# Kernel optimization log

Hardware: AMD Instinct MI355X
Metric: run time of the kernel (lower is better)

The kernel has to match this reference:

```python
import jax, jax.numpy as jnp
import numpy as np


def setup_inputs() -> dict:
    key = jax.random.key(0)
    k = jax.random.split(key, 5)
    B, S, D, H = 4, 2048, 2048, 8192
    scale1 = 1.0 / np.sqrt(D)
    scale2 = 1.0 / np.sqrt(H)
    return {
        "x": jax.random.normal(k[0], (B, S, D), dtype=jnp.float32),
        "w1": jax.random.normal(k[1], (H, D), dtype=jnp.float32) * scale1,
        "b1": jax.random.normal(k[2], (H,), dtype=jnp.float32) * scale1,
        "w2": jax.random.normal(k[3], (D, H), dtype=jnp.float32) * scale2,
        "b2": jax.random.normal(k[4], (D,), dtype=jnp.float32) * scale2,
    }


def reference(x, w1, b1, w2, b2):
    # fc1: [B,S,D] @ [D,H] -> [B,S,H]
    h = jnp.einsum("bsd,hd->bsh", x, w1) + b1
    # squared ReLU activation
    a = jnp.square(jax.nn.relu(h))
    # fc2: [B,S,H] @ [H,D] -> [B,S,D]
    return jnp.einsum("bsh,dh->bsd", a, w2) + b2
```

## Files before the change

### kernel.cpp

```cpp
#include <hip/hip_runtime.h>
#include <hip/hip_bf16.h>
#include <stdint.h>

typedef __bf16 bf16x8 __attribute__((ext_vector_type(8)));
typedef float f32x4 __attribute__((ext_vector_type(4)));


__device__ inline void gload_lds16(const void* g, void* lds) {
  __builtin_amdgcn_global_load_lds(
      (const __attribute__((address_space(1))) uint32_t*)(uintptr_t)g,
      (__attribute__((address_space(3))) uint32_t*)(uintptr_t)lds,
      16, 0, 0);
}

#define DSR(dst, base, OFF)                                         \
  asm volatile("ds_read_b128 %0, %1 offset:" #OFF                   \
               : "=v"(dst) : "v"(base))

#define LGKM(N) do {                                             \
    asm volatile("s_waitcnt lgkmcnt(" #N ")" ::: "memory");      \
    __builtin_amdgcn_sched_barrier(0);                           \
  } while (0)
#define VM(N) do {                                               \
    asm volatile("s_waitcnt vmcnt(" #N ")" ::: "memory");        \
    __builtin_amdgcn_sched_barrier(0);                           \
  } while (0)

__device__ inline short f2bf(float f) {
  union { float f; uint32_t u; } x; x.f = f;
  uint32_t u = x.u;
  u += 0x7fffu + ((u >> 16) & 1u);
  return (short)(u >> 16);
}

#define BAR() do { asm volatile("" ::: "memory"); \
                   __builtin_amdgcn_s_barrier();  \
                   asm volatile("" ::: "memory"); } while (0)


__global__ __launch_bounds__(256) void cvt_f32_bf16(
    const float* __restrict__ in, short* __restrict__ out, int n4) {
  int i = blockIdx.x * 256 + threadIdx.x;
  if (i < n4) {
    float4 v = reinterpret_cast<const float4*>(in)[i];
    short4 o;
    o.x = f2bf(v.x); o.y = f2bf(v.y); o.z = f2bf(v.z); o.w = f2bf(v.w);
    reinterpret_cast<short4*>(out)[i] = o;
  }
}


template <int EPI>
__global__ __launch_bounds__(512, 2) void gemm_bt(
    const short* __restrict__ A, const short* __restrict__ B,
    const float* __restrict__ bias, void* __restrict__ Cout,
    int M, int N, int K) {
  __shared__ __align__(16) short lds[2][4][128 * 64];

  const int tid  = threadIdx.x;
  const int wave = tid >> 6;
  const int lane = tid & 63;
  const int wr = wave >> 2;
  const int wc = wave & 3;
  const int fr = lane & 15, kq = lane >> 4;

  const int nwg = gridDim.x;
  const int w = (blockIdx.x & 7) * (nwg >> 3) + (blockIdx.x >> 3);
  const int gy = M >> 8;
  const int brow = w % gy;
  const int bcol = w / gy;

  f32x4 acc[8][4];
#pragma unroll
  for (int m = 0; m < 8; ++m)
#pragma unroll
    for (int n = 0; n < 4; ++n)
      acc[m][n] = (f32x4){0.f, 0.f, 0.f, 0.f};

  const int nk = K >> 6;

  const uint32_t LB = (uint32_t)(uintptr_t)&lds[0][0][0];
  uint32_t bA[2], bB[2];
  {
    const uint32_t x0 = (uint32_t)(((kq)     ^ (fr & 7)) * 16);
    const uint32_t x1 = (uint32_t)(((4 + kq) ^ (fr & 7)) * 16);
    const uint32_t ra = (uint32_t)((wr * 64 + fr) * 128);
    const uint32_t rb = (uint32_t)((wc * 32 + fr) * 128);
    bA[0] = LB + ra + x0;            bA[1] = LB + ra + x1;
    bB[0] = LB + 32768u + rb + x0;   bB[1] = LB + 32768u + rb + x1;
  }

  const int i0 = tid;
  const int gl0 = i0 ^ ((i0 >> 3) & 7);
  const int r0 = gl0 >> 3, c0 = gl0 & 7;
  const size_t rstep = (size_t)128 * K;

  const short* pA[2];
  const short* pB[2];
  {
    const int rb0 = (r0 >> 5) * 64 + (r0 & 31);
#pragma unroll
    for (int h = 0; h < 2; ++h) {
      pA[h] = A + (size_t)(brow * 256 + h * 64 + r0) * K + c0 * 8;
      pB[h] = B + (size_t)(bcol * 256 + rb0 + h * 32) * K + c0 * 8;
    }
  }

  const int dst0 = wave * 512, dst1 = 4096 + wave * 512;

#define STAGE(p, buf, slot)                              \
  do {                                                   \
    short* base_ = &lds[buf][slot][0];                   \
    gload_lds16((p), base_ + dst0);                      \
    gload_lds16((p) + rstep, base_ + dst1);              \
    (p) += 64;                                           \
  } while (0)

  bf16x8 a0q[4][2], a1q[4][2], bq0[2][2], bq1[2][2];
  auto Q1 = [&]() {
#pragma unroll
    for (int m = 0; m < 4; ++m)
#pragma unroll
      for (int n = 0; n < 2; ++n)
#pragma unroll
        for (int kk = 0; kk < 2; ++kk)
          acc[m][n] = __builtin_amdgcn_mfma_f32_16x16x32_bf16(
              bq0[n][kk], a0q[m][kk], acc[m][n], 0, 0, 0);
  };
  auto Q2 = [&]() {
#pragma unroll
    for (int m = 0; m < 4; ++m)
#pragma unroll
      for (int n = 0; n < 2; ++n)
#pragma unroll
        for (int kk = 0; kk < 2; ++kk)
          acc[m][n + 2] = __builtin_amdgcn_mfma_f32_16x16x32_bf16(
              bq1[n][kk], a0q[m][kk], acc[m][n + 2], 0, 0, 0);
  };
  auto Q3 = [&]() {
#pragma unroll
    for (int m = 0; m < 4; ++m)
#pragma unroll
      for (int n = 0; n < 2; ++n)
#pragma unroll
        for (int kk = 0; kk < 2; ++kk)
          acc[m + 4][n + 2] = __builtin_amdgcn_mfma_f32_16x16x32_bf16(
              bq1[n][kk], a1q[m][kk], acc[m + 4][n + 2], 0, 0, 0);
  };
  auto Q4 = [&]() {
#pragma unroll
    for (int m = 0; m < 4; ++m)
#pragma unroll
      for (int n = 0; n < 2; ++n)
#pragma unroll
        for (int kk = 0; kk < 2; ++kk)
          acc[m + 4][n] = __builtin_amdgcn_mfma_f32_16x16x32_bf16(
              bq0[n][kk], a1q[m][kk], acc[m + 4][n], 0, 0, 0);
  };

#define PRIO_ON  __builtin_amdgcn_s_setprio(1)
#define PRIO_OFF __builtin_amdgcn_s_setprio(0)

  STAGE(pA[0], 0, 0);
  STAGE(pB[0], 0, 2);
  STAGE(pB[1], 0, 3);
  STAGE(pA[1], 0, 1);
  STAGE(pA[0], 1, 0);
  STAGE(pB[0], 1, 2);
  STAGE(pB[1], 1, 3);
  VM(6);
  BAR();

  for (int t = 0; t < nk; ++t) {
    const int cur = t & 1, nxt = cur ^ 1;
    const bool s1 = (t + 1) < nk, g2 = (t + 2) < nk;
    if (t) {
      const int32_t d = cur ? 65536 : -65536;
      bA[0] += d; bA[1] += d; bB[0] += d; bB[1] += d;
    }

    DSR(a0q[0][0], bA[0], 0);     DSR(a0q[0][1], bA[1], 0);
    DSR(a0q[1][0], bA[0], 2048);  DSR(a0q[1][1], bA[1], 2048);
    DSR(a0q[2][0], bA[0], 4096);  DSR(a0q[2][1], bA[1], 4096);
    DSR(a0q[3][0], bA[0], 6144);  DSR(a0q[3][1], bA[1], 6144);
    DSR(bq0[0][0], bB[0], 0);     DSR(bq0[0][1], bB[1], 0);
    DSR(bq0[1][0], bB[0], 2048);  DSR(bq0[1][1], bB[1], 2048);
    if (s1) STAGE(pA[1], nxt, 1);
    LGKM(8);
    BAR();
    LGKM(0);
    PRIO_ON; Q1(); PRIO_OFF;
    BAR();

    DSR(bq1[0][0], bB[0], 16384); DSR(bq1[0][1], bB[1], 16384);
    DSR(bq1[1][0], bB[0], 18432); DSR(bq1[1][1], bB[1], 18432);
    if (g2) STAGE(pA[0], cur, 0);
    BAR();
    LGKM(0);
    PRIO_ON; Q2(); PRIO_OFF;
    BAR();

    DSR(a1q[0][0], bA[0], 16384); DSR(a1q[0][1], bA[1], 16384);
    DSR(a1q[1][0], bA[0], 18432); DSR(a1q[1][1], bA[1], 18432);
    DSR(a1q[2][0], bA[0], 20480); DSR(a1q[2][1], bA[1], 20480);
    DSR(a1q[3][0], bA[0], 22528); DSR(a1q[3][1], bA[1], 22528);
    if (g2) STAGE(pB[0], cur, 2);
    BAR();
    LGKM(0);
    PRIO_ON; Q3(); PRIO_OFF;
    BAR();

    if (g2) STAGE(pB[1], cur, 3);
    BAR();
    PRIO_ON; Q4(); PRIO_OFF;
    if (g2)      { VM(6); }
    else if (s1) { VM(0); }
    if (s1) BAR();
  }

  const int q = lane >> 4;
  if (EPI == 0) {
    short* C = (short*)Cout;
#pragma unroll
    for (int m = 0; m < 8; ++m) {
      const int row = brow * 256 + wr * 128 + m * 16 + fr;
#pragma unroll
      for (int n = 0; n < 4; ++n) {
        const int col = bcol * 256 + wc * 64 + n * 16 + q * 4;
        const float4 bv = *(const float4*)&bias[col];
        short4 o;
        float v0 = acc[m][n][0] + bv.x; v0 = v0 > 0.f ? v0 * v0 : 0.f;
        float v1 = acc[m][n][1] + bv.y; v1 = v1 > 0.f ? v1 * v1 : 0.f;
        float v2 = acc[m][n][2] + bv.z; v2 = v2 > 0.f ? v2 * v2 : 0.f;
        float v3 = acc[m][n][3] + bv.w; v3 = v3 > 0.f ? v3 * v3 : 0.f;
        o.x = f2bf(v0); o.y = f2bf(v1); o.z = f2bf(v2); o.w = f2bf(v3);
        *(short4*)&C[(size_t)row * N + col] = o;
      }
    }
  } else {
    float* C = (float*)Cout;
#pragma unroll
    for (int m = 0; m < 8; ++m) {
      const int row = brow * 256 + wr * 128 + m * 16 + fr;
#pragma unroll
      for (int n = 0; n < 4; ++n) {
        const int col = bcol * 256 + wc * 64 + n * 16 + q * 4;
        const float4 bv = *(const float4*)&bias[col];
        float4 o;
        o.x = acc[m][n][0] + bv.x;
        o.y = acc[m][n][1] + bv.y;
        o.z = acc[m][n][2] + bv.z;
        o.w = acc[m][n][3] + bv.w;
        *(float4*)&C[(size_t)row * N + col] = o;
      }
    }
  }
#undef STAGE
}


extern "C" void kernel_launch(void* const* d_in, const int* in_sizes, int n_in,
                              void* d_out, int out_size, void* d_ws,
                              size_t ws_size, hipStream_t stream) {
  const float* x  = (const float*)d_in[0];
  const float* w1 = (const float*)d_in[1];
  const float* b1 = (const float*)d_in[2];
  const float* w2 = (const float*)d_in[3];
  const float* b2 = (const float*)d_in[4];
  float* out = (float*)d_out;

  const int H = in_sizes[2];
  const int D = in_sizes[4];
  const int M = in_sizes[0] / D;

  short* xb  = (short*)d_ws;
  short* w1b = xb  + (size_t)M * D;
  short* w2b = w1b + (size_t)H * D;
  short* act = w2b + (size_t)D * H;

  {
    int n4 = (M * D) / 4;
    cvt_f32_bf16<<<(n4 + 255) / 256, 256, 0, stream>>>(x, xb, n4);
    n4 = (H * D) / 4;
    cvt_f32_bf16<<<(n4 + 255) / 256, 256, 0, stream>>>(w1, w1b, n4);
    n4 = (D * H) / 4;
    cvt_f32_bf16<<<(n4 + 255) / 256, 256, 0, stream>>>(w2, w2b, n4);
  }

  gemm_bt<0><<<(M / 256) * (H / 256), 512, 0, stream>>>(
      xb, w1b, b1, (void*)act, M, H, D);
  gemm_bt<1><<<(M / 256) * (D / 256), 512, 0, stream>>>(
      act, w2b, b2, (void*)out, M, D, H);
}
```

Before: 547.9 us.

## Unroll GEMM main loop by two with cross-iteration LDS fragment prefetch

Restructures the double-buffered bf16 MFMA main loop into a two-way unrolled loop with ping-pong register sets, so the first A/B fragments of the next K-tile are read from LDS during the last quadrant of the current tile. It uses fixed per-buffer LDS base addresses instead of runtime toggling, and moves global-to-LDS staging and vmcnt waits into a uniform schedule with a peeled tail. The aim is to hide LDS read latency behind MFMA work and cut per-iteration branch and address arithmetic. The cost is more VGPRs for the extra fragment set, which may lower occupancy. The loop also assumes an even number of K-tiles.

```diff
diff --git a/kernel.cpp b/kernel.cpp
--- a/kernel.cpp
+++ b/kernel.cpp
@@ -80,14 +80,16 @@
   const int nk = K >> 6;
 
   const uint32_t LB = (uint32_t)(uintptr_t)&lds[0][0][0];
-  uint32_t bA[2], bB[2];
+  uint32_t bA0[2], bB0[2], bA1[2], bB1[2];
   {
     const uint32_t x0 = (uint32_t)(((kq)     ^ (fr & 7)) * 16);
     const uint32_t x1 = (uint32_t)(((4 + kq) ^ (fr & 7)) * 16);
     const uint32_t ra = (uint32_t)((wr * 64 + fr) * 128);
     const uint32_t rb = (uint32_t)((wc * 32 + fr) * 128);
-    bA[0] = LB + ra + x0;            bA[1] = LB + ra + x1;
-    bB[0] = LB + 32768u + rb + x0;   bB[1] = LB + 32768u + rb + x1;
+    bA0[0] = LB + ra + x0;            bA0[1] = LB + ra + x1;
+    bB0[0] = LB + 32768u + rb + x0;   bB0[1] = LB + 32768u + rb + x1;
+    bA1[0] = bA0[0] + 65536u;         bA1[1] = bA0[1] + 65536u;
+    bB1[0] = bB0[0] + 65536u;         bB1[1] = bB0[1] + 65536u;
   }
 
   const int i0 = tid;
@@ -116,8 +118,30 @@
     (p) += 64;                                           \
   } while (0)
 
-  bf16x8 a0q[4][2], a1q[4][2], bq0[2][2], bq1[2][2];
-  auto Q1 = [&]() {
+  bf16x8 a0X[4][2], b0X[2][2], a0Y[4][2], b0Y[2][2];
+  bf16x8 a1q[4][2], b1q[2][2];
+
+  auto PRE = [&](bf16x8 (&aS)[4][2], bf16x8 (&bS)[2][2],
+                 const uint32_t* bA_, const uint32_t* bB_) {
+    DSR(aS[0][0], bA_[0], 0);     DSR(aS[0][1], bA_[1], 0);
+    DSR(aS[1][0], bA_[0], 2048);  DSR(aS[1][1], bA_[1], 2048);
+    DSR(aS[2][0], bA_[0], 4096);  DSR(aS[2][1], bA_[1], 4096);
+    DSR(aS[3][0], bA_[0], 6144);  DSR(aS[3][1], bA_[1], 6144);
+    DSR(bS[0][0], bB_[0], 0);     DSR(bS[0][1], bB_[1], 0);
+    DSR(bS[1][0], bB_[0], 2048);  DSR(bS[1][1], bB_[1], 2048);
+  };
+  auto RDB1 = [&](const uint32_t* bB_) {
+    DSR(b1q[0][0], bB_[0], 16384); DSR(b1q[0][1], bB_[1], 16384);
+    DSR(b1q[1][0], bB_[0], 18432); DSR(b1q[1][1], bB_[1], 18432);
+  };
+  auto RDA1 = [&](const uint32_t* bA_) {
+    DSR(a1q[0][0], bA_[0], 16384); DSR(a1q[0][1], bA_[1], 16384);
+    DSR(a1q[1][0], bA_[0], 18432); DSR(a1q[1][1], bA_[1], 18432);
+    DSR(a1q[2][0], bA_[0], 20480); DSR(a1q[2][1], bA_[1], 20480);
+    DSR(a1q[3][0], bA_[0], 22528); DSR(a1q[3][1], bA_[1], 22528);
+  };
+
+  auto Q1 = [&](bf16x8 (&aS)[4][2], bf16x8 (&bS)[2][2]) {
 #pragma unroll
     for (int m = 0; m < 4; ++m)
 #pragma unroll
@@ -125,9 +149,9 @@
 #pragma unroll
         for (int kk = 0; kk < 2; ++kk)
           acc[m][n] = __builtin_amdgcn_mfma_f32_16x16x32_bf16(
-              bq0[n][kk], a0q[m][kk], acc[m][n], 0, 0, 0);
-  };
-  auto Q2 = [&]() {
+              bS[n][kk], aS[m][kk], acc[m][n], 0, 0, 0);
+  };
+  auto Q2 = [&](bf16x8 (&aS)[4][2]) {
 #pragma unroll
     for (int m = 0; m < 4; ++m)
 #pragma unroll
@@ -135,7 +159,7 @@
 #pragma unroll
         for (int kk = 0; kk < 2; ++kk)
           acc[m][n + 2] = __builtin_amdgcn_mfma_f32_16x16x32_bf16(
-              bq1[n][kk], a0q[m][kk], acc[m][n + 2], 0, 0, 0);
+              b1q[n][kk], aS[m][kk], acc[m][n + 2], 0, 0, 0);
   };
   auto Q3 = [&]() {
 #pragma unroll
@@ -145,9 +169,9 @@
 #pragma unroll
         for (int kk = 0; kk < 2; ++kk)
           acc[m + 4][n + 2] = __builtin_amdgcn_mfma_f32_16x16x32_bf16(
-              bq1[n][kk], a1q[m][kk], acc[m + 4][n + 2], 0, 0, 0);
-  };
-  auto Q4 = [&]() {
+              b1q[n][kk], a1q[m][kk], acc[m + 4][n + 2], 0, 0, 0);
+  };
+  auto Q4 = [&](bf16x8 (&bS)[2][2]) {
 #pragma unroll
     for (int m = 0; m < 4; ++m)
 #pragma unroll
@@ -155,7 +179,7 @@
 #pragma unroll
         for (int kk = 0; kk < 2; ++kk)
           acc[m + 4][n] = __builtin_amdgcn_mfma_f32_16x16x32_bf16(
-              bq0[n][kk], a1q[m][kk], acc[m + 4][n], 0, 0, 0);
+              bS[n][kk], a1q[m][kk], acc[m + 4][n], 0, 0, 0);
   };
 
 #define PRIO_ON  __builtin_amdgcn_s_setprio(1)
@@ -170,53 +194,75 @@
   STAGE(pB[1], 1, 3);
   VM(6);
   BAR();
-
-  for (int t = 0; t < nk; ++t) {
-    const int cur = t & 1, nxt = cur ^ 1;
-    const bool s1 = (t + 1) < nk, g2 = (t + 2) < nk;
-    if (t) {
-      const int32_t d = cur ? 65536 : -65536;
-      bA[0] += d; bA[1] += d; bB[0] += d; bB[1] += d;
-    }
-
-    DSR(a0q[0][0], bA[0], 0);     DSR(a0q[0][1], bA[1], 0);
-    DSR(a0q[1][0], bA[0], 2048);  DSR(a0q[1][1], bA[1], 2048);
-    DSR(a0q[2][0], bA[0], 4096);  DSR(a0q[2][1], bA[1], 4096);
-    DSR(a0q[3][0], bA[0], 6144);  DSR(a0q[3][1], bA[1], 6144);
-    DSR(bq0[0][0], bB[0], 0);     DSR(bq0[0][1], bB[1], 0);
-    DSR(bq0[1][0], bB[0], 2048);  DSR(bq0[1][1], bB[1], 2048);
-    if (s1) STAGE(pA[1], nxt, 1);
+  PRE(a0X, b0X, bA0, bB0);
+
+  const int niter = nk >> 1;
+  for (int i = 0; i < niter - 1; ++i) {
+    RDB1(bB0);  STAGE(pA[1], 1, 1);
+    BAR(); LGKM(4);
+    PRIO_ON; Q1(a0X, b0X); PRIO_OFF;
+    VM(8); BAR();
+    RDA1(bA0);  STAGE(pA[0], 0, 0);
+    BAR(); LGKM(8);
+    PRIO_ON; Q2(a0X); PRIO_OFF;
+    VM(8); BAR();
+    STAGE(pB[0], 0, 2);
+    BAR(); LGKM(0);
+    PRIO_ON; Q3(); PRIO_OFF;
+    VM(8); BAR();
+    PRE(a0Y, b0Y, bA1, bB1);  STAGE(pB[1], 0, 3);
     LGKM(8);
-    BAR();
-    LGKM(0);
-    PRIO_ON; Q1(); PRIO_OFF;
-    BAR();
-
-    DSR(bq1[0][0], bB[0], 16384); DSR(bq1[0][1], bB[1], 16384);
-    DSR(bq1[1][0], bB[0], 18432); DSR(bq1[1][1], bB[1], 18432);
-    if (g2) STAGE(pA[0], cur, 0);
-    BAR();
-    LGKM(0);
-    PRIO_ON; Q2(); PRIO_OFF;
-    BAR();
-
-    DSR(a1q[0][0], bA[0], 16384); DSR(a1q[0][1], bA[1], 16384);
-    DSR(a1q[1][0], bA[0], 18432); DSR(a1q[1][1], bA[1], 18432);
-    DSR(a1q[2][0], bA[0], 20480); DSR(a1q[2][1], bA[1], 20480);
-    DSR(a1q[3][0], bA[0], 22528); DSR(a1q[3][1], bA[1], 22528);
-    if (g2) STAGE(pB[0], cur, 2);
-    BAR();
-    LGKM(0);
+    BAR(); __builtin_amdgcn_sched_barrier(0);
+    PRIO_ON; Q4(b0X); PRIO_OFF;
+    VM(8); BAR();
+
+    RDB1(bB1);  STAGE(pA[1], 0, 1);
+    BAR(); LGKM(4);
+    PRIO_ON; Q1(a0Y, b0Y); PRIO_OFF;
+    VM(8); BAR();
+    RDA1(bA1);  STAGE(pA[0], 1, 0);
+    BAR(); LGKM(8);
+    PRIO_ON; Q2(a0Y); PRIO_OFF;
+    VM(8); BAR();
+    STAGE(pB[0], 1, 2);
+    BAR(); LGKM(0);
     PRIO_ON; Q3(); PRIO_OFF;
-    BAR();
-
-    if (g2) STAGE(pB[1], cur, 3);
-    BAR();
-    PRIO_ON; Q4(); PRIO_OFF;
-    if (g2)      { VM(6); }
-    else if (s1) { VM(0); }
-    if (s1) BAR();
-  }
+    VM(8); BAR();
+    PRE(a0X, b0X, bA0, bB0);  STAGE(pB[1], 1, 3);
+    LGKM(8);
+    BAR(); __builtin_amdgcn_sched_barrier(0);
+    PRIO_ON; Q4(b0Y); PRIO_OFF;
+    VM(8); BAR();
+  }
+
+  RDB1(bB0);  STAGE(pA[1], 1, 1);
+  BAR(); LGKM(4);
+  PRIO_ON; Q1(a0X, b0X); PRIO_OFF;
+  VM(0); BAR();
+  RDA1(bA0);
+  BAR(); LGKM(8);
+  PRIO_ON; Q2(a0X); PRIO_OFF;
+  BAR();
+  BAR(); LGKM(0);
+  PRIO_ON; Q3(); PRIO_OFF;
+  BAR();
+  PRE(a0Y, b0Y, bA1, bB1);
+  LGKM(8);
+  BAR(); __builtin_amdgcn_sched_barrier(0);
+  PRIO_ON; Q4(b0X); PRIO_OFF;
+  BAR();
+  RDB1(bB1);
+  BAR(); LGKM(4);
+  PRIO_ON; Q1(a0Y, b0Y); PRIO_OFF;
+  BAR();
+  RDA1(bA1);
+  BAR(); LGKM(8);
+  PRIO_ON; Q2(a0Y); PRIO_OFF;
+  BAR();
+  BAR(); LGKM(0);
+  PRIO_ON; Q3(); PRIO_OFF;
+  BAR();
+  PRIO_ON; Q4(b0Y); PRIO_OFF;
 
   const int q = lane >> 4;
   if (EPI == 0) {
```

After: 2.183 ms. 3.98x slower.

## Use 4-wave 256-thread GEMM blocks with 128x128 per-wave tiles and unrolled double-buffer loop

Applied to the files above, without the earlier changes.

Cuts the GEMM workgroup from 8 waves to 4. Each wave now computes a 128x128 output tile (8x8 accumulators) instead of 128x64, which raises register reuse of LDS fragments per MFMA. The main loop is unrolled by two over the double buffer so buffer indices and LDS addresses are constants, and a peeled epilogue drains the pipeline with explicit vmcnt waits. Each wave now issues four global-to-LDS loads per stage, and the doubled accumulator set with occupancy bound 1 risks register spills and less latency hiding.

```diff
diff --git a/kernel.cpp b/kernel.cpp
--- a/kernel.cpp
+++ b/kernel.cpp
@@ -51,7 +51,7 @@
 
 
 template <int EPI>
-__global__ __launch_bounds__(512, 2) void gemm_bt(
+__global__ __launch_bounds__(256, 1) void gemm_bt(
     const short* __restrict__ A, const short* __restrict__ B,
     const float* __restrict__ bias, void* __restrict__ Cout,
     int M, int N, int K) {
@@ -60,8 +60,8 @@
   const int tid  = threadIdx.x;
   const int wave = tid >> 6;
   const int lane = tid & 63;
-  const int wr = wave >> 2;
-  const int wc = wave & 3;
+  const int wr = wave >> 1;
+  const int wc = wave & 1;
   const int fr = lane & 15, kq = lane >> 4;
 
   const int nwg = gridDim.x;
@@ -70,58 +70,58 @@
   const int brow = w % gy;
   const int bcol = w / gy;
 
-  f32x4 acc[8][4];
+  f32x4 acc[8][8];
 #pragma unroll
   for (int m = 0; m < 8; ++m)
 #pragma unroll
-    for (int n = 0; n < 4; ++n)
+    for (int n = 0; n < 8; ++n)
       acc[m][n] = (f32x4){0.f, 0.f, 0.f, 0.f};
 
   const int nk = K >> 6;
 
   const uint32_t LB = (uint32_t)(uintptr_t)&lds[0][0][0];
-  uint32_t bA[2], bB[2];
+  uint32_t bA0[2], bB0[2], bA1b[2], bB1b[2];
   {
     const uint32_t x0 = (uint32_t)(((kq)     ^ (fr & 7)) * 16);
     const uint32_t x1 = (uint32_t)(((4 + kq) ^ (fr & 7)) * 16);
     const uint32_t ra = (uint32_t)((wr * 64 + fr) * 128);
-    const uint32_t rb = (uint32_t)((wc * 32 + fr) * 128);
-    bA[0] = LB + ra + x0;            bA[1] = LB + ra + x1;
-    bB[0] = LB + 32768u + rb + x0;   bB[1] = LB + 32768u + rb + x1;
-  }
-
-  const int i0 = tid;
-  const int gl0 = i0 ^ ((i0 >> 3) & 7);
+    const uint32_t rb = (uint32_t)((wc * 64 + fr) * 128);
+    bA0[0] = LB + ra + x0;            bA0[1] = LB + ra + x1;
+    bB0[0] = LB + 32768u + rb + x0;   bB0[1] = LB + 32768u + rb + x1;
+    bA1b[0] = bA0[0] + 65536u;        bA1b[1] = bA0[1] + 65536u;
+    bB1b[0] = bB0[0] + 65536u;        bB1b[1] = bB0[1] + 65536u;
+  }
+
+  const int gl0 = (tid ^ ((tid >> 3) & 7)) & 255;
   const int r0 = gl0 >> 3, c0 = gl0 & 7;
-  const size_t rstep = (size_t)128 * K;
 
   const short* pA[2];
   const short* pB[2];
-  {
-    const int rb0 = (r0 >> 5) * 64 + (r0 & 31);
-#pragma unroll
-    for (int h = 0; h < 2; ++h) {
-      pA[h] = A + (size_t)(brow * 256 + h * 64 + r0) * K + c0 * 8;
-      pB[h] = B + (size_t)(bcol * 256 + rb0 + h * 32) * K + c0 * 8;
-    }
-  }
-
-  const int dst0 = wave * 512, dst1 = 4096 + wave * 512;
-
-#define STAGE(p, buf, slot)                              \
-  do {                                                   \
-    short* base_ = &lds[buf][slot][0];                   \
-    gload_lds16((p), base_ + dst0);                      \
-    gload_lds16((p) + rstep, base_ + dst1);              \
-    (p) += 64;                                           \
+#pragma unroll
+  for (int s = 0; s < 2; ++s) {
+    pA[s] = A + (size_t)(brow * 256 + s * 64 + r0) * K + c0 * 8;
+    pB[s] = B + (size_t)(bcol * 256 + s * 64 + r0) * K + c0 * 8;
+  }
+  const size_t rk32 = (size_t)32 * K, rk128 = (size_t)128 * K;
+  const size_t rk160 = (size_t)160 * K;
+  const int dstw = wave * 512;
+
+#define STAGE(p, buf, slot)                                       \
+  do {                                                            \
+    short* base_ = &lds[buf][slot][0];                            \
+    gload_lds16((p),          base_ + dstw);                      \
+    gload_lds16((p) + rk32,   base_ + 2048 + dstw);               \
+    gload_lds16((p) + rk128,  base_ + 4096 + dstw);               \
+    gload_lds16((p) + rk160,  base_ + 6144 + dstw);               \
+    (p) += 64;                                                    \
   } while (0)
 
-  bf16x8 a0q[4][2], a1q[4][2], bq0[2][2], bq1[2][2];
+  bf16x8 a0q[4][2], a1q[4][2], bq0[4][2], bq1[4][2];
   auto Q1 = [&]() {
 #pragma unroll
     for (int m = 0; m < 4; ++m)
 #pragma unroll
-      for (int n = 0; n < 2; ++n)
+      for (int n = 0; n < 4; ++n)
 #pragma unroll
         for (int kk = 0; kk < 2; ++kk)
           acc[m][n] = __builtin_amdgcn_mfma_f32_16x16x32_bf16(
@@ -131,31 +131,55 @@
 #pragma unroll
     for (int m = 0; m < 4; ++m)
 #pragma unroll
-      for (int n = 0; n < 2; ++n)
+      for (int n = 0; n < 4; ++n)
 #pragma unroll
         for (int kk = 0; kk < 2; ++kk)
-          acc[m][n + 2] = __builtin_amdgcn_mfma_f32_16x16x32_bf16(
-              bq1[n][kk], a0q[m][kk], acc[m][n + 2], 0, 0, 0);
+          acc[m][n + 4] = __builtin_amdgcn_mfma_f32_16x16x32_bf16(
+              bq1[n][kk], a0q[m][kk], acc[m][n + 4], 0, 0, 0);
   };
   auto Q3 = [&]() {
 #pragma unroll
     for (int m = 0; m < 4; ++m)
 #pragma unroll
-      for (int n = 0; n < 2; ++n)
+      for (int n = 0; n < 4; ++n)
 #pragma unroll
         for (int kk = 0; kk < 2; ++kk)
-          acc[m + 4][n + 2] = __builtin_amdgcn_mfma_f32_16x16x32_bf16(
-              bq1[n][kk], a1q[m][kk], acc[m + 4][n + 2], 0, 0, 0);
+          acc[m + 4][n + 4] = __builtin_amdgcn_mfma_f32_16x16x32_bf16(
+              bq1[n][kk], a1q[m][kk], acc[m + 4][n + 4], 0, 0, 0);
   };
   auto Q4 = [&]() {
 #pragma unroll
     for (int m = 0; m < 4; ++m)
 #pragma unroll
-      for (int n = 0; n < 2; ++n)
+      for (int n = 0; n < 4; ++n)
 #pragma unroll
         for (int kk = 0; kk < 2; ++kk)
           acc[m + 4][n] = __builtin_amdgcn_mfma_f32_16x16x32_bf16(
               bq0[n][kk], a1q[m][kk], acc[m + 4][n], 0, 0, 0);
+  };
+  auto RD_A0 = [&](const uint32_t* bA_) {
+    DSR(a0q[0][0], bA_[0], 0);     DSR(a0q[0][1], bA_[1], 0);
+    DSR(a0q[1][0], bA_[0], 2048);  DSR(a0q[1][1], bA_[1], 2048);
+    DSR(a0q[2][0], bA_[0], 4096);  DSR(a0q[2][1], bA_[1], 4096);
+    DSR(a0q[3][0], bA_[0], 6144);  DSR(a0q[3][1], bA_[1], 6144);
+  };
+  auto RD_B0 = [&](const uint32_t* bB_) {
+    DSR(bq0[0][0], bB_[0], 0);     DSR(bq0[0][1], bB_[1], 0);
+    DSR(bq0[1][0], bB_[0], 2048);  DSR(bq0[1][1], bB_[1], 2048);
+    DSR(bq0[2][0], bB_[0], 4096);  DSR(bq0[2][1], bB_[1], 4096);
+    DSR(bq0[3][0], bB_[0], 6144);  DSR(bq0[3][1], bB_[1], 6144);
+  };
+  auto RD_B1 = [&](const uint32_t* bB_) {
+    DSR(bq1[0][0], bB_[0], 16384); DSR(bq1[0][1], bB_[1], 16384);
+    DSR(bq1[1][0], bB_[0], 18432); DSR(bq1[1][1], bB_[1], 18432);
+    DSR(bq1[2][0], bB_[0], 20480); DSR(bq1[2][1], bB_[1], 20480);
+    DSR(bq1[3][0], bB_[0], 22528); DSR(bq1[3][1], bB_[1], 22528);
+  };
+  auto RD_A1 = [&](const uint32_t* bA_) {
+    DSR(a1q[0][0], bA_[0], 16384); DSR(a1q[0][1], bA_[1], 16384);
+    DSR(a1q[1][0], bA_[0], 18432); DSR(a1q[1][1], bA_[1], 18432);
+    DSR(a1q[2][0], bA_[0], 20480); DSR(a1q[2][1], bA_[1], 20480);
+    DSR(a1q[3][0], bA_[0], 22528); DSR(a1q[3][1], bA_[1], 22528);
   };
 
 #define PRIO_ON  __builtin_amdgcn_s_setprio(1)
@@ -168,55 +192,78 @@
   STAGE(pA[0], 1, 0);
   STAGE(pB[0], 1, 2);
   STAGE(pB[1], 1, 3);
-  VM(6);
+  VM(12);
   BAR();
 
-  for (int t = 0; t < nk; ++t) {
-    const int cur = t & 1, nxt = cur ^ 1;
-    const bool s1 = (t + 1) < nk, g2 = (t + 2) < nk;
-    if (t) {
-      const int32_t d = cur ? 65536 : -65536;
-      bA[0] += d; bA[1] += d; bB[0] += d; bB[1] += d;
-    }
-
-    DSR(a0q[0][0], bA[0], 0);     DSR(a0q[0][1], bA[1], 0);
-    DSR(a0q[1][0], bA[0], 2048);  DSR(a0q[1][1], bA[1], 2048);
-    DSR(a0q[2][0], bA[0], 4096);  DSR(a0q[2][1], bA[1], 4096);
-    DSR(a0q[3][0], bA[0], 6144);  DSR(a0q[3][1], bA[1], 6144);
-    DSR(bq0[0][0], bB[0], 0);     DSR(bq0[0][1], bB[1], 0);
-    DSR(bq0[1][0], bB[0], 2048);  DSR(bq0[1][1], bB[1], 2048);
-    if (s1) STAGE(pA[1], nxt, 1);
+  const int niter = nk >> 1;
+  for (int i = 0; i < niter - 1; ++i) {
+    RD_A0(bA0); RD_B0(bB0);  STAGE(pA[1], 1, 1);
     LGKM(8);
-    BAR();
-    LGKM(0);
+    BAR(); LGKM(0);
     PRIO_ON; Q1(); PRIO_OFF;
-    BAR();
-
-    DSR(bq1[0][0], bB[0], 16384); DSR(bq1[0][1], bB[1], 16384);
-    DSR(bq1[1][0], bB[0], 18432); DSR(bq1[1][1], bB[1], 18432);
-    if (g2) STAGE(pA[0], cur, 0);
-    BAR();
-    LGKM(0);
+    VM(20); BAR();
+    RD_B1(bB0);  STAGE(pA[0], 0, 0);
+    BAR(); LGKM(0);
     PRIO_ON; Q2(); PRIO_OFF;
-    BAR();
-
-    DSR(a1q[0][0], bA[0], 16384); DSR(a1q[0][1], bA[1], 16384);
-    DSR(a1q[1][0], bA[0], 18432); DSR(a1q[1][1], bA[1], 18432);
-    DSR(a1q[2][0], bA[0], 20480); DSR(a1q[2][1], bA[1], 20480);
-    DSR(a1q[3][0], bA[0], 22528); DSR(a1q[3][1], bA[1], 22528);
-    if (g2) STAGE(pB[0], cur, 2);
-    BAR();
-    LGKM(0);
+    VM(20); BAR();
+    RD_A1(bA0);  STAGE(pB[0], 0, 2);
+    BAR(); LGKM(0);
     PRIO_ON; Q3(); PRIO_OFF;
-    BAR();
-
-    if (g2) STAGE(pB[1], cur, 3);
+    VM(20); BAR();
+    STAGE(pB[1], 0, 3);
     BAR();
     PRIO_ON; Q4(); PRIO_OFF;
-    if (g2)      { VM(6); }
-    else if (s1) { VM(0); }
-    if (s1) BAR();
-  }
+    VM(20); BAR();
+
+    RD_A0(bA1b); RD_B0(bB1b);  STAGE(pA[1], 0, 1);
+    LGKM(8);
+    BAR(); LGKM(0);
+    PRIO_ON; Q1(); PRIO_OFF;
+    VM(20); BAR();
+    RD_B1(bB1b);  STAGE(pA[0], 1, 0);
+    BAR(); LGKM(0);
+    PRIO_ON; Q2(); PRIO_OFF;
+    VM(20); BAR();
+    RD_A1(bA1b);  STAGE(pB[0], 1, 2);
+    BAR(); LGKM(0);
+    PRIO_ON; Q3(); PRIO_OFF;
+    VM(20); BAR();
+    STAGE(pB[1], 1, 3);
+    BAR();
+    PRIO_ON; Q4(); PRIO_OFF;
+    VM(20); BAR();
+  }
+
+  RD_A0(bA0); RD_B0(bB0);  STAGE(pA[1], 1, 1);
+  LGKM(8);
+  BAR(); LGKM(0);
+  PRIO_ON; Q1(); PRIO_OFF;
+  VM(20); BAR();
+  RD_B1(bB0);
+  BAR(); LGKM(0);
+  PRIO_ON; Q2(); PRIO_OFF;
+  VM(16); BAR();
+  RD_A1(bA0);
+  BAR(); LGKM(0);
+  PRIO_ON; Q3(); PRIO_OFF;
+  VM(12); BAR();
+  BAR();
+  PRIO_ON; Q4(); PRIO_OFF;
+  VM(8); BAR();
+  RD_A0(bA1b); RD_B0(bB1b);
+  LGKM(8);
+  BAR(); LGKM(0);
+  PRIO_ON; Q1(); PRIO_OFF;
+  VM(4); BAR();
+  RD_B1(bB1b);
+  BAR(); LGKM(0);
+  PRIO_ON; Q2(); PRIO_OFF;
+  VM(0); BAR();
+  RD_A1(bA1b);
+  BAR(); LGKM(0);
+  PRIO_ON; Q3(); PRIO_OFF;
+  BAR();
+  PRIO_ON; Q4(); PRIO_OFF;
 
   const int q = lane >> 4;
   if (EPI == 0) {
@@ -225,8 +272,8 @@
     for (int m = 0; m < 8; ++m) {
       const int row = brow * 256 + wr * 128 + m * 16 + fr;
 #pragma unroll
-      for (int n = 0; n < 4; ++n) {
-        const int col = bcol * 256 + wc * 64 + n * 16 + q * 4;
+      for (int n = 0; n < 8; ++n) {
+        const int col = bcol * 256 + wc * 128 + n * 16 + q * 4;
         const float4 bv = *(const float4*)&bias[col];
         short4 o;
         float v0 = acc[m][n][0] + bv.x; v0 = v0 > 0.f ? v0 * v0 : 0.f;
@@ -243,8 +290,8 @@
     for (int m = 0; m < 8; ++m) {
       const int row = brow * 256 + wr * 128 + m * 16 + fr;
 #pragma unroll
-      for (int n = 0; n < 4; ++n) {
-        const int col = bcol * 256 + wc * 64 + n * 16 + q * 4;
+      for (int n = 0; n < 8; ++n) {
+        const int col = bcol * 256 + wc * 128 + n * 16 + q * 4;
         const float4 bv = *(const float4*)&bias[col];
         float4 o;
         o.x = acc[m][n][0] + bv.x;
@@ -287,8 +334,8 @@
     cvt_f32_bf16<<<(n4 + 255) / 256, 256, 0, stream>>>(w2, w2b, n4);
   }
 
-  gemm_bt<0><<<(M / 256) * (H / 256), 512, 0, stream>>>(
+  gemm_bt<0><<<(M / 256) * (H / 256), 256, 0, stream>>>(
       xb, w1b, b1, (void*)act, M, H, D);
-  gemm_bt<1><<<(M / 256) * (D / 256), 512, 0, stream>>>(
+  gemm_bt<1><<<(M / 256) * (D / 256), 256, 0, stream>>>(
       act, w2b, b2, (void*)out, M, D, H);
 }
```

Measured after the change: 624.1 us. +13.9%, slower.
